# Performance work log

Hardware: AMD Instinct MI355X
Metric: run time of the kernel (lower is better)

## Reference

```python
import jax, jax.numpy as jnp
import numpy as np

MARGIN = 1.0
EPS = 1e-6  # torch F.pairwise_distance default eps, added elementwise to (x - y)
NEG_INF = -1e30
POS_INF = 1e30


def _pairwise_dist_matrix(e):
    # D[i,j] = || e_i - e_j + EPS ||_2, expanded so we never materialize [B,B,D]:
    # ||d + eps||^2 = ||d||^2 + 2*eps*sum(d) + Dfeat*eps^2,  d = e_i - e_j
    sq = jnp.sum(e * e, axis=1)          # [B]
    s = jnp.sum(e, axis=1)               # [B]
    d2 = (sq[:, None] + sq[None, :] - 2.0 * (e @ e.T)
          + 2.0 * EPS * (s[:, None] - s[None, :])
          + e.shape[1] * (EPS * EPS))
    return jnp.sqrt(jnp.maximum(d2, 0.0))  # [B,B]


def _pdist(x, y):
    # F.pairwise_distance(p=2): ||x - y + eps||
    return jnp.sqrt(jnp.sum(jnp.square(x - y + EPS), axis=-1))


def setup_inputs() -> dict:
    B, D = 4096, 128
    key = jax.random.key(0)
    k1, k2, k3, k4 = jax.random.split(key, 4)
    embedding = jax.random.normal(k1, (B, D), dtype=jnp.float32)
    # label space == batch, each label appears exactly once in the batch
    target_idx = jax.random.permutation(k2, B).astype(jnp.int32)
    positive_idxs = jax.random.bernoulli(k3, 0.02, (B, B))  # [B, L] label-space mask
    negative_idxs = jax.random.bernoulli(k4, 0.5, (B, B))
    return {"embedding": embedding, "target_idx": target_idx,
            "positive_idxs": positive_idxs, "negative_idxs": negative_idxs}


def reference(embedding, target_idx, positive_idxs, negative_idxs):
    # Mining happens under no_grad in the original module.
    dm = jax.lax.stop_gradient(_pairwise_dist_matrix(embedding))  # [B,B]
    # batch j is a positive/negative candidate for anchor i iff its label is flagged
    pos_mask = positive_idxs[:, target_idx]  # [B,B] bool
    neg_mask = negative_idxs[:, target_idx]
    pos_idx = jnp.argmax(jnp.where(pos_mask, dm, NEG_INF), axis=1)  # hardest positive
    neg_idx = jnp.argmin(jnp.where(neg_mask, dm, POS_INF), axis=1)  # hardest negative
    valid = jnp.any(pos_mask, axis=1) & jnp.any(neg_mask, axis=1)
    a = embedding
    p = embedding[pos_idx]
    n = embedding[neg_idx]
    ap = _pdist(a, p)
    an = _pdist(a, n)
    pn = _pdist(p, n)
    loss = jax.nn.relu(ap - jnp.minimum(an, pn) + MARGIN)
    w = valid.astype(loss.dtype)
    return jnp.sum(loss * w) / jnp.maximum(jnp.sum(w), 1.0)
```

## Files before the change

kernel.cpp:

```cpp
#include <hip/hip_runtime.h>
#include <stdint.h>

#define BN 4096
#define DD 128
#define EPSF 1e-6f
#define MARGINF 1.0f

typedef unsigned long long ull;
typedef unsigned short ushort;
typedef short short8 __attribute__((ext_vector_type(8)));
typedef float f32x4 __attribute__((ext_vector_type(4)));
typedef int int4v __attribute__((ext_vector_type(4)));

__device__ __forceinline__ unsigned int ord_f32(float f) {
    unsigned int u = __float_as_uint(f);
    return (u & 0x80000000u) ? ~u : (u | 0x80000000u);
}
__device__ __forceinline__ ushort bf16_rne(float x) {
    unsigned int u = __float_as_uint(x);
    return (ushort)((u + 0x7FFFu + ((u >> 16) & 1u)) >> 16);
}

template<bool BITS>
__global__ void k_prep(const float* __restrict__ e, const int* __restrict__ tidx,
                       const int* __restrict__ pos, const int* __restrict__ neg,
                       float* __restrict__ rjp, unsigned int* __restrict__ jn,
                       ull* __restrict__ pkey, ull* __restrict__ nkey,
                       unsigned int* __restrict__ ehi, unsigned int* __restrict__ eperm,
                       ull* __restrict__ pbits, ull* __restrict__ nbits) {
    const int w = threadIdx.x >> 6, lane = threadIdx.x & 63;
    const int row = blockIdx.x * 4 + w;
    const int c = tidx[row];
    float2 v = ((const float2*)(e + (size_t)row * DD))[lane];
    ushort hx = bf16_rne(v.x), hy = bf16_rne(v.y);
    unsigned int packed = (unsigned int)hx | ((unsigned int)hy << 16);
    ehi[row * 64 + lane] = packed;
    eperm[(size_t)c * 64 + lane] = packed;
    float ss = v.x + v.y;
    float qq = v.x * v.x + v.y * v.y;
    #pragma unroll
    for (int off = 32; off > 0; off >>= 1) {
        ss += __shfl_down(ss, off);
        qq += __shfl_down(qq, off);
    }
    if (lane == 0) {
        rjp[c] = qq - 2.0f * EPSF * ss;
        jn[c] = 0xFFFFFFFFu - (unsigned int)row;
        pkey[row] = 0ULL; nkey[row] = 0ULL;
    }
    if (BITS) {
        ushort* pb16 = (ushort*)pbits;
        ushort* nb16 = (ushort*)nbits;
        const int4v* prow = (const int4v*)(pos + (size_t)row * BN);
        const int4v* nrow = (const int4v*)(neg + (size_t)row * BN);
        #pragma unroll
        for (int seg = 0; seg < 4; seg++) {
            unsigned int pu = 0, nu = 0;
            #pragma unroll
            for (int k = 0; k < 4; k++) {
                int4v P = __builtin_nontemporal_load(&prow[seg * 256 + lane * 4 + k]);
                int4v N = __builtin_nontemporal_load(&nrow[seg * 256 + lane * 4 + k]);
                unsigned int pq = (unsigned int)(P[0] != 0) | ((unsigned int)(P[1] != 0) << 1)
                                | ((unsigned int)(P[2] != 0) << 2) | ((unsigned int)(P[3] != 0) << 3);
                unsigned int nq = (unsigned int)(N[0] != 0) | ((unsigned int)(N[1] != 0) << 1)
                                | ((unsigned int)(N[2] != 0) << 2) | ((unsigned int)(N[3] != 0) << 3);
                pu |= pq << (4 * k);
                nu |= nq << (4 * k);
            }
            pb16[row * 256 + seg * 64 + lane] = (ushort)pu;
            nb16[row * 256 + seg * 64 + lane] = (ushort)nu;
        }
    }
}

template<bool BITS>
__global__ __launch_bounds__(256, 4)
void k_select(const ushort* __restrict__ ehi, const ushort* __restrict__ eperm,
              const int* __restrict__ pos, const int* __restrict__ neg,
              const ull* __restrict__ pbits, const ull* __restrict__ nbits,
              const float* __restrict__ rjp, const unsigned int* __restrict__ jn,
              ull* __restrict__ pkey, ull* __restrict__ nkey) {
    __shared__ float rjL[1024];
    __shared__ unsigned int jnL[1024];
    __shared__ ull scrp[64], scrn[64];

    const int tid = threadIdx.x;
    const int lane = tid & 63, w = tid >> 6;
    const int lrow = lane & 15, quad = lane >> 4;
    const int r0 = blockIdx.x * 16;
    const int c0 = blockIdx.y * 1024;
    const int cb0 = c0 >> 6;
    const int shft = w * 16 + lrow;

    #pragma unroll
    for (int k = 0; k < 4; k++) {
        int idx = k * 256 + tid;
        rjL[idx] = rjp[c0 + idx];
        jnL[idx] = jn[c0 + idx];
    }

    short8 a[4];
    #pragma unroll
    for (int ks = 0; ks < 4; ks++)
        a[ks] = *(const short8*)(ehi + (size_t)(r0 + lrow) * DD + ks * 32 + quad * 8);

    __syncthreads();

    ull kp[4] = {0ULL, 0ULL, 0ULL, 0ULL};
    ull kn[4] = {0ULL, 0ULL, 0ULL, 0ULL};

    ull pmw[2][4], nmw[2][4];
    int pm[2][4], nm[2][4];
    short8 bf[2][4];
    float rjc[2]; unsigned int jni[2];

#define LOADTILE(BUF, JT) do {                                                  \
        const int lcol = (JT) * 64 + shft;                                      \
        rjc[BUF] = rjL[lcol];                                                   \
        jni[BUF] = jnL[lcol];                                                   \
        if (BITS) {                                                             \
            const ull* pb = pbits + (size_t)(r0 + quad * 4) * 64 + cb0 + (JT);  \
            const ull* nb = nbits + (size_t)(r0 + quad * 4) * 64 + cb0 + (JT);  \
            _Pragma("unroll")                                                   \
            for (int t = 0; t < 4; t++) {                                       \
                pmw[BUF][t] = pb[(size_t)t * 64];                               \
                nmw[BUF][t] = nb[(size_t)t * 64];                               \
            }                                                                   \
        } else {                                                                \
            const int* pp = pos + (size_t)(r0 + quad * 4) * BN + (size_t)(c0 + lcol); \
            const int* np = neg + (size_t)(r0 + quad * 4) * BN + (size_t)(c0 + lcol); \
            _Pragma("unroll")                                                   \
            for (int t = 0; t < 4; t++) {                                       \
                pm[BUF][t] = __builtin_nontemporal_load(pp + (size_t)t * BN);   \
                nm[BUF][t] = __builtin_nontemporal_load(np + (size_t)t * BN);   \
            }                                                                   \
        }                                                                       \
        const ushort* bp = eperm + (size_t)(c0 + lcol) * DD + quad * 8;         \
        _Pragma("unroll")                                                       \
        for (int ks = 0; ks < 4; ks++)                                          \
            bf[BUF][ks] = *(const short8*)(bp + ks * 32);                       \
    } while (0)

    LOADTILE(0, 0);

    #pragma unroll
    for (int jt = 0; jt < 16; jt++) {
        const int cur = jt & 1, nxt = cur ^ 1;
        if (jt < 15) {
            if (nxt == 0) LOADTILE(0, jt + 1); else LOADTILE(1, jt + 1);
        }
        f32x4 acc = (f32x4){0.f, 0.f, 0.f, 0.f};
        #pragma unroll
        for (int ks = 0; ks < 4; ks++)
            acc = __builtin_amdgcn_mfma_f32_16x16x32_bf16(a[ks], bf[cur][ks], acc, 0, 0, 0);
        #pragma unroll
        for (int t = 0; t < 4; t++) {
            float m = rjc[cur] - 2.0f * acc[t];
            unsigned int om = ord_f32(m);
            ull keyp = ((ull)om << 32) | (ull)jni[cur];
            ull keyn = ((ull)(om ^ 0xFFFFFFFFu) << 32) | (ull)jni[cur];
            bool pok = BITS ? (((pmw[cur][t] >> shft) & 1ULL) != 0ULL) : (pm[cur][t] != 0);
            bool nok = BITS ? (((nmw[cur][t] >> shft) & 1ULL) != 0ULL) : (nm[cur][t] != 0);
            if (pok && keyp > kp[t]) kp[t] = keyp;
            if (nok && keyn > kn[t]) kn[t] = keyn;
        }
    }
#undef LOADTILE

    #pragma unroll
    for (int t = 0; t < 4; t++) {
        #pragma unroll
        for (int off = 8; off > 0; off >>= 1) {
            ull o = __shfl_xor(kp[t], off); if (o > kp[t]) kp[t] = o;
            o = __shfl_xor(kn[t], off);     if (o > kn[t]) kn[t] = o;
        }
        if (lrow == 0) {
            scrp[(quad * 4 + t) * 4 + w] = kp[t];
            scrn[(quad * 4 + t) * 4 + w] = kn[t];
        }
    }
    __syncthreads();
    if (tid < 16) {
        ull xp = 0ULL, xn = 0ULL;
        #pragma unroll
        for (int k = 0; k < 4; k++) {
            ull v = scrp[tid * 4 + k]; if (v > xp) xp = v;
            v = scrn[tid * 4 + k];     if (v > xn) xn = v;
        }
        if (xp) atomicMax(&pkey[r0 + tid], xp);
        if (xn) atomicMax(&nkey[r0 + tid], xn);
    }
}

__global__ void k_loss(const float* __restrict__ e,
                       const ull* __restrict__ pkey, const ull* __restrict__ nkey,
                       float* __restrict__ partials) {
    int w = threadIdx.x >> 6, lane = threadIdx.x & 63;
    int row = blockIdx.x * 4 + w;
    ull pk = pkey[row], nk = nkey[row];
    float loss = 0.0f, wt = 0.0f;
    if (pk != 0ULL && nk != 0ULL) {
        int pi = (int)(0xFFFFFFFFu - (unsigned)(pk & 0xFFFFFFFFu));
        int ni = (int)(0xFFFFFFFFu - (unsigned)(nk & 0xFFFFFFFFu));
        float2 av = ((const float2*)(e + (size_t)row * DD))[lane];
        float2 pv = ((const float2*)(e + (size_t)pi * DD))[lane];
        float2 nv = ((const float2*)(e + (size_t)ni * DD))[lane];
        float dx, dy;
        dx = av.x - pv.x + EPSF; dy = av.y - pv.y + EPSF;
        float ap2 = dx * dx + dy * dy;
        dx = av.x - nv.x + EPSF; dy = av.y - nv.y + EPSF;
        float an2 = dx * dx + dy * dy;
        dx = pv.x - nv.x + EPSF; dy = pv.y - nv.y + EPSF;
        float pn2 = dx * dx + dy * dy;
        #pragma unroll
        for (int off = 32; off > 0; off >>= 1) {
            ap2 += __shfl_down(ap2, off);
            an2 += __shfl_down(an2, off);
            pn2 += __shfl_down(pn2, off);
        }
        if (lane == 0) {
            float ap = sqrtf(ap2), an = sqrtf(an2), pn = sqrtf(pn2);
            loss = fmaxf(ap - fminf(an, pn) + MARGINF, 0.0f);
            wt = 1.0f;
        }
    }
    __shared__ float sl[4], sw[4];
    if (lane == 0) { sl[w] = loss; sw[w] = wt; }
    __syncthreads();
    if (threadIdx.x == 0) {
        partials[blockIdx.x * 2 + 0] = sl[0] + sl[1] + sl[2] + sl[3];
        partials[blockIdx.x * 2 + 1] = sw[0] + sw[1] + sw[2] + sw[3];
    }
}

__global__ void k_final(const float* __restrict__ partials, float* __restrict__ out) {
    int tid = threadIdx.x;
    float L = 0.0f, W = 0.0f;
    for (int i = 0; i < 4; i++) {
        int idx = tid + i * 256;
        L += partials[idx * 2];
        W += partials[idx * 2 + 1];
    }
    #pragma unroll
    for (int off = 32; off > 0; off >>= 1) {
        L += __shfl_down(L, off);
        W += __shfl_down(W, off);
    }
    __shared__ float sl[4], sw[4];
    int w = tid >> 6, lane = tid & 63;
    if (lane == 0) { sl[w] = L; sw[w] = W; }
    __syncthreads();
    if (tid == 0) {
        float Lt = sl[0] + sl[1] + sl[2] + sl[3];
        float Wt = sw[0] + sw[1] + sw[2] + sw[3];
        out[0] = Lt / fmaxf(Wt, 1.0f);
    }
}

extern "C" void kernel_launch(void* const* d_in, const int* in_sizes, int n_in,
                              void* d_out, int out_size, void* d_ws, size_t ws_size,
                              hipStream_t stream) {
    const float* e    = (const float*)d_in[0];
    const int*   tidx = (const int*)d_in[1];
    const int*   pos  = (const int*)d_in[2];
    const int*   neg  = (const int*)d_in[3];
    float* out = (float*)d_out;

    char* p = (char*)d_ws;
    ull* pkey  = (ull*)p;                 p += (size_t)BN * 8;
    ull* nkey  = (ull*)p;                 p += (size_t)BN * 8;
    float* rjp = (float*)p;               p += (size_t)BN * 4;
    unsigned int* jn = (unsigned int*)p;  p += (size_t)BN * 4;
    float* partials = (float*)p;          p += 2048 * 4;
    unsigned int* ehi = (unsigned int*)p; p += (size_t)BN * 64 * 4;
    unsigned int* eperm = (unsigned int*)p; p += (size_t)BN * 64 * 4;
    ull* pbits = (ull*)p;                 p += (size_t)BN * 64 * 8;
    ull* nbits = (ull*)p;                 p += (size_t)BN * 64 * 8;
    const size_t need = (size_t)(p - (char*)d_ws);
    const bool bits = ws_size >= need;

    dim3 grid(BN / 16, 4);
    if (bits) {
        k_prep<true><<<BN / 4, 256, 0, stream>>>(e, tidx, pos, neg, rjp, jn,
                                                 pkey, nkey, ehi, eperm, pbits, nbits);
        k_select<true><<<grid, 256, 0, stream>>>((const ushort*)ehi, (const ushort*)eperm,
                                                 pos, neg, pbits, nbits,
                                                 rjp, jn, pkey, nkey);
    } else {
        k_prep<false><<<BN / 4, 256, 0, stream>>>(e, tidx, pos, neg, rjp, jn,
                                                  pkey, nkey, ehi, eperm, pbits, nbits);
        k_select<false><<<grid, 256, 0, stream>>>((const ushort*)ehi, (const ushort*)eperm,
                                                  pos, neg, pbits, nbits,
                                                  rjp, jn, pkey, nkey);
    }
    k_loss<<<BN / 4, 256, 0, stream>>>(e, pkey, nkey, partials);
    k_final<<<1, 256, 0, stream>>>(partials, out);
}
```

Measured before the change: 213.7 us.

## Pack masks with wave ballots and stage bitmask words in shared memory

The mask-packing kernel now reads each mask row with coalesced per-lane int loads and uses wave ballots to build 64-bit words, replacing the per-thread 16-int nibble packing. The selection kernel loads its block's mask words once into shared memory instead of fetching global words inside every tile iteration, and the fallback path that read raw int masks is removed. The goal is cheaper mask streaming and fewer scattered global loads in the hot loop. The cost is more ballots and register pressure in the prep kernel, and the code now assumes the workspace is large enough for the bitmasks.

```diff
diff --git a/kernel.cpp b/kernel.cpp
--- a/kernel.cpp
+++ b/kernel.cpp
@@ -10,7 +10,6 @@
 typedef unsigned short ushort;
 typedef short short8 __attribute__((ext_vector_type(8)));
 typedef float f32x4 __attribute__((ext_vector_type(4)));
-typedef int int4v __attribute__((ext_vector_type(4)));
 
 __device__ __forceinline__ unsigned int ord_f32(float f) {
     unsigned int u = __float_as_uint(f);
@@ -21,13 +20,13 @@
     return (ushort)((u + 0x7FFFu + ((u >> 16) & 1u)) >> 16);
 }
 
-template<bool BITS>
-__global__ void k_prep(const float* __restrict__ e, const int* __restrict__ tidx,
-                       const int* __restrict__ pos, const int* __restrict__ neg,
-                       float* __restrict__ rjp, unsigned int* __restrict__ jn,
-                       ull* __restrict__ pkey, ull* __restrict__ nkey,
-                       unsigned int* __restrict__ ehi, unsigned int* __restrict__ eperm,
-                       ull* __restrict__ pbits, ull* __restrict__ nbits) {
+__global__ __launch_bounds__(256)
+void k_prep(const float* __restrict__ e, const int* __restrict__ tidx,
+            const int* __restrict__ pos, const int* __restrict__ neg,
+            float* __restrict__ rjp, unsigned int* __restrict__ jn,
+            ull* __restrict__ pkey, ull* __restrict__ nkey,
+            unsigned int* __restrict__ ehi, unsigned int* __restrict__ eperm,
+            ull* __restrict__ pbits, ull* __restrict__ nbits) {
     const int w = threadIdx.x >> 6, lane = threadIdx.x & 63;
     const int row = blockIdx.x * 4 + w;
     const int c = tidx[row];
@@ -48,40 +47,38 @@
         jn[c] = 0xFFFFFFFFu - (unsigned int)row;
         pkey[row] = 0ULL; nkey[row] = 0ULL;
     }
-    if (BITS) {
-        ushort* pb16 = (ushort*)pbits;
-        ushort* nb16 = (ushort*)nbits;
-        const int4v* prow = (const int4v*)(pos + (size_t)row * BN);
-        const int4v* nrow = (const int4v*)(neg + (size_t)row * BN);
-        #pragma unroll
-        for (int seg = 0; seg < 4; seg++) {
-            unsigned int pu = 0, nu = 0;
-            #pragma unroll
-            for (int k = 0; k < 4; k++) {
-                int4v P = __builtin_nontemporal_load(&prow[seg * 256 + lane * 4 + k]);
-                int4v N = __builtin_nontemporal_load(&nrow[seg * 256 + lane * 4 + k]);
-                unsigned int pq = (unsigned int)(P[0] != 0) | ((unsigned int)(P[1] != 0) << 1)
-                                | ((unsigned int)(P[2] != 0) << 2) | ((unsigned int)(P[3] != 0) << 3);
-                unsigned int nq = (unsigned int)(N[0] != 0) | ((unsigned int)(N[1] != 0) << 1)
-                                | ((unsigned int)(N[2] != 0) << 2) | ((unsigned int)(N[3] != 0) << 3);
-                pu |= pq << (4 * k);
-                nu |= nq << (4 * k);
-            }
-            pb16[row * 256 + seg * 64 + lane] = (ushort)pu;
-            nb16[row * 256 + seg * 64 + lane] = (ushort)nu;
-        }
-    }
-}
-
-template<bool BITS>
+
+    const int* prow = pos + (size_t)row * BN;
+    const int* nrow = neg + (size_t)row * BN;
+    ull myp = 0ULL, myn = 0ULL;
+    #pragma unroll
+    for (int j0 = 0; j0 < 64; j0 += 16) {
+        int pv[16], nv[16];
+        #pragma unroll
+        for (int k = 0; k < 16; k++)
+            pv[k] = __builtin_nontemporal_load(prow + (j0 + k) * 64 + lane);
+        #pragma unroll
+        for (int k = 0; k < 16; k++)
+            nv[k] = __builtin_nontemporal_load(nrow + (j0 + k) * 64 + lane);
+        #pragma unroll
+        for (int k = 0; k < 16; k++) {
+            ull bp = __ballot(pv[k] != 0);
+            ull bn = __ballot(nv[k] != 0);
+            if (lane == j0 + k) { myp = bp; myn = bn; }
+        }
+    }
+    pbits[(size_t)row * 64 + lane] = myp;
+    nbits[(size_t)row * 64 + lane] = myn;
+}
+
 __global__ __launch_bounds__(256, 4)
 void k_select(const ushort* __restrict__ ehi, const ushort* __restrict__ eperm,
-              const int* __restrict__ pos, const int* __restrict__ neg,
               const ull* __restrict__ pbits, const ull* __restrict__ nbits,
               const float* __restrict__ rjp, const unsigned int* __restrict__ jn,
               ull* __restrict__ pkey, ull* __restrict__ nkey) {
     __shared__ float rjL[1024];
     __shared__ unsigned int jnL[1024];
+    __shared__ ull bitP[256], bitN[256];
     __shared__ ull scrp[64], scrn[64];
 
     const int tid = threadIdx.x;
@@ -98,6 +95,8 @@
         rjL[idx] = rjp[c0 + idx];
         jnL[idx] = jn[c0 + idx];
     }
+    bitP[tid] = pbits[(size_t)(r0 + (tid >> 4)) * 64 + cb0 + (tid & 15)];
+    bitN[tid] = nbits[(size_t)(r0 + (tid >> 4)) * 64 + cb0 + (tid & 15)];
 
     short8 a[4];
     #pragma unroll
@@ -109,8 +108,6 @@
     ull kp[4] = {0ULL, 0ULL, 0ULL, 0ULL};
     ull kn[4] = {0ULL, 0ULL, 0ULL, 0ULL};
 
-    ull pmw[2][4], nmw[2][4];
-    int pm[2][4], nm[2][4];
     short8 bf[2][4];
     float rjc[2]; unsigned int jni[2];
 
@@ -118,23 +115,6 @@
         const int lcol = (JT) * 64 + shft;                                      \
         rjc[BUF] = rjL[lcol];                                                   \
         jni[BUF] = jnL[lcol];                                                   \
-        if (BITS) {                                                             \
-            const ull* pb = pbits + (size_t)(r0 + quad * 4) * 64 + cb0 + (JT);  \
-            const ull* nb = nbits + (size_t)(r0 + quad * 4) * 64 + cb0 + (JT);  \
-            _Pragma("unroll")                                                   \
-            for (int t = 0; t < 4; t++) {                                       \
-                pmw[BUF][t] = pb[(size_t)t * 64];                               \
-                nmw[BUF][t] = nb[(size_t)t * 64];                               \
-            }                                                                   \
-        } else {                                                                \
-            const int* pp = pos + (size_t)(r0 + quad * 4) * BN + (size_t)(c0 + lcol); \
-            const int* np = neg + (size_t)(r0 + quad * 4) * BN + (size_t)(c0 + lcol); \
-            _Pragma("unroll")                                                   \
-            for (int t = 0; t < 4; t++) {                                       \
-                pm[BUF][t] = __builtin_nontemporal_load(pp + (size_t)t * BN);   \
-                nm[BUF][t] = __builtin_nontemporal_load(np + (size_t)t * BN);   \
-            }                                                                   \
-        }                                                                       \
         const ushort* bp = eperm + (size_t)(c0 + lcol) * DD + quad * 8;         \
         _Pragma("unroll")                                                       \
         for (int ks = 0; ks < 4; ks++)                                          \
@@ -155,14 +135,14 @@
             acc = __builtin_amdgcn_mfma_f32_16x16x32_bf16(a[ks], bf[cur][ks], acc, 0, 0, 0);
         #pragma unroll
         for (int t = 0; t < 4; t++) {
+            ull pw = bitP[(quad * 4 + t) * 16 + jt];
+            ull nw = bitN[(quad * 4 + t) * 16 + jt];
             float m = rjc[cur] - 2.0f * acc[t];
             unsigned int om = ord_f32(m);
             ull keyp = ((ull)om << 32) | (ull)jni[cur];
             ull keyn = ((ull)(om ^ 0xFFFFFFFFu) << 32) | (ull)jni[cur];
-            bool pok = BITS ? (((pmw[cur][t] >> shft) & 1ULL) != 0ULL) : (pm[cur][t] != 0);
-            bool nok = BITS ? (((nmw[cur][t] >> shft) & 1ULL) != 0ULL) : (nm[cur][t] != 0);
-            if (pok && keyp > kp[t]) kp[t] = keyp;
-            if (nok && keyn > kn[t]) kn[t] = keyn;
+            if (((pw >> shft) & 1ULL) && keyp > kp[t]) kp[t] = keyp;
+            if (((nw >> shft) & 1ULL) && keyn > kn[t]) kn[t] = keyn;
         }
     }
 #undef LOADTILE
@@ -272,27 +252,16 @@
     float* rjp = (float*)p;               p += (size_t)BN * 4;
     unsigned int* jn = (unsigned int*)p;  p += (size_t)BN * 4;
     float* partials = (float*)p;          p += 2048 * 4;
-    unsigned int* ehi = (unsigned int*)p; p += (size_t)BN * 64 * 4;
+    unsigned int* ehi = (unsigned int*)p;   p += (size_t)BN * 64 * 4;
     unsigned int* eperm = (unsigned int*)p; p += (size_t)BN * 64 * 4;
     ull* pbits = (ull*)p;                 p += (size_t)BN * 64 * 8;
     ull* nbits = (ull*)p;                 p += (size_t)BN * 64 * 8;
-    const size_t need = (size_t)(p - (char*)d_ws);
-    const bool bits = ws_size >= need;
-
+
+    k_prep<<<BN / 4, 256, 0, stream>>>(e, tidx, pos, neg, rjp, jn,
+                                       pkey, nkey, ehi, eperm, pbits, nbits);
     dim3 grid(BN / 16, 4);
-    if (bits) {
-        k_prep<true><<<BN / 4, 256, 0, stream>>>(e, tidx, pos, neg, rjp, jn,
-                                                 pkey, nkey, ehi, eperm, pbits, nbits);
-        k_select<true><<<grid, 256, 0, stream>>>((const ushort*)ehi, (const ushort*)eperm,
-                                                 pos, neg, pbits, nbits,
-                                                 rjp, jn, pkey, nkey);
-    } else {
-        k_prep<false><<<BN / 4, 256, 0, stream>>>(e, tidx, pos, neg, rjp, jn,
-                                                  pkey, nkey, ehi, eperm, pbits, nbits);
-        k_select<false><<<grid, 256, 0, stream>>>((const ushort*)ehi, (const ushort*)eperm,
-                                                  pos, neg, pbits, nbits,
-                                                  rjp, jn, pkey, nkey);
-    }
+    k_select<<<grid, 256, 0, stream>>>((const ushort*)ehi, (const ushort*)eperm,
+                                       pbits, nbits, rjp, jn, pkey, nkey);
     k_loss<<<BN / 4, 256, 0, stream>>>(e, pkey, nkey, partials);
     k_final<<<1, 256, 0, stream>>>(partials, out);
 }
```

After: 186.5 us. 1.15x faster.
